# Optimization experiments

Measured on AMD Instinct MI355X. Metric: run time of the kernel, lower is better.

## Reference

```python
import jax, jax.numpy as jnp
import numpy as np

B, L, H, D = 4, 2048, 8, 64


def _combined_mask(Lq):
    # True = masked (disallowed), matching masked_fill_(mask, -inf)
    i = jnp.arange(Lq)[:, None]
    j = jnp.arange(Lq)[None, :]
    diff = i - j
    # log-sparse: query i attends to itself and positions at power-of-2 offsets back
    pow2 = (diff > 0) & ((diff & (diff - 1)) == 0)
    allowed = (diff == 0) | pow2
    log_mask = ~allowed
    causal = j > i  # TriangularCausalMask: strictly-upper triangle masked
    return log_mask | causal  # [Lq, Lq]


def setup_inputs() -> dict:
    key = jax.random.key(0)
    kq, kk, kv = jax.random.split(key, 3)
    return {
        "queries": jax.random.normal(kq, (B, L, H, D), jnp.float32),
        "keys": jax.random.normal(kk, (B, L, H, D), jnp.float32),
        "values": jax.random.normal(kv, (B, L, H, D), jnp.float32),
    }


def reference(queries, keys, values):
    Bq, Lq, Hh, Dd = queries.shape
    scale = 1.0 / jnp.sqrt(jnp.asarray(Dd, queries.dtype))
    # dense scores [B,H,L,L], then structured log-sparse + causal masking
    scores = jnp.einsum('blhd,bshd->bhls', queries, keys)
    mask = _combined_mask(Lq)  # [L,L] True = masked
    scores = jnp.where(mask[None, None, :, :], -jnp.inf, scores)
    A = jax.nn.softmax(scale * scores, axis=-1)  # scale*(-inf) stays -inf
    # dropout is identity in eval mode (reference baseline)
    V = jnp.einsum('bhls,bshd->blhd', A, values)
    return V
```

## Files before the change

kernel.cpp:

```cpp
#include <hip/hip_runtime.h>


typedef float f32x4 __attribute__((ext_vector_type(4)));

constexpr int B = 4, L = 2048, H = 8, D = 64;
constexpr int STRIP = 32, WIN = 32, LROWS = STRIP + WIN;
constexpr int NWG = B * H * (L / STRIP);

__global__ __launch_bounds__(256) void logsparse_attn_kernel(
    const float* __restrict__ Qg, const float* __restrict__ Kg,
    const float* __restrict__ Vg, float* __restrict__ Og) {
  __shared__ float Ks[LROWS * D];
  __shared__ float Vs[LROWS * D];

  const int bid   = blockIdx.x;
  const int xcd   = bid & 7;
  const int kk    = bid >> 3;
  const int bh    = xcd * 4 + (kk >> 6);
  const int strip = kk & 63;
  const int b = bh >> 3, h = bh & 7;
  const int s = strip * STRIP;

  const int tid  = threadIdx.x;
  const int w    = tid >> 6;
  const int lane = tid & 63;
  const int sub  = lane >> 4;
  const int dl   = lane & 15;

  f32x4 kreg[4], vreg[4];
  int dst[4];
  #pragma unroll
  for (int q = 0; q < 4; ++q) {
    const int r  = w * 16 + q * 4 + sub;
    const int j  = s - WIN + r;
    const int jc = j < 0 ? 0 : j;
    const uint32_t src = (((uint32_t)(b * L + jc)) * H + h) * D + dl * 4;
    kreg[q] = *(const f32x4*)(Kg + src);
    vreg[q] = *(const f32x4*)(Vg + src);
    dst[q]  = r * D + dl * 4;
  }
  #pragma unroll
  for (int q = 0; q < 4; ++q) {
    *(f32x4*)&Ks[dst[q]] = kreg[q];
    *(f32x4*)&Vs[dst[q]] = vreg[q];
  }
  __syncthreads();

  const float qs = 0.125f * 1.4426950408889634f;

  #pragma unroll
  for (int p = 0; p < 2; ++p) {
    const int il = w * 8 + p * 4 + sub;
    const int i  = s + il;
    const uint32_t qb = (((uint32_t)(b * L + i)) * H + h) * D + dl * 4;
    f32x4 q4 = *(const f32x4*)(Qg + qb);

    f32x4 kfar[5], vfar[5];
    #pragma unroll
    for (int t = 0; t < 5; ++t) {
      const int off = 64 << t;
      const int jc  = (off <= i) ? (i - off) : 0;
      const uint32_t rb = (((uint32_t)(b * L + jc)) * H + h) * D + dl * 4;
      kfar[t] = *(const f32x4*)(Kg + rb);
      vfar[t] = *(const f32x4*)(Vg + rb);
    }

    q4.x *= qs; q4.y *= qs; q4.z *= qs; q4.w *= qs;

    float sc[12];
    #pragma unroll
    for (int t = 0; t < 7; ++t) {
      const int off = (t == 0) ? 0 : (1 << (t - 1));
      const int r   = il + WIN - off;
      const f32x4 k4 = *(const f32x4*)&Ks[r * D + dl * 4];
      float pp = q4.x * k4.x + q4.y * k4.y + q4.z * k4.z + q4.w * k4.w;
      pp += __shfl_xor(pp, 1, 64);
      pp += __shfl_xor(pp, 2, 64);
      pp += __shfl_xor(pp, 4, 64);
      pp += __shfl_xor(pp, 8, 64);
      sc[t] = (off <= i) ? pp : -1e30f;
    }
    #pragma unroll
    for (int t = 0; t < 5; ++t) {
      const int off = 64 << t;
      float pp = q4.x * kfar[t].x + q4.y * kfar[t].y
               + q4.z * kfar[t].z + q4.w * kfar[t].w;
      pp += __shfl_xor(pp, 1, 64);
      pp += __shfl_xor(pp, 2, 64);
      pp += __shfl_xor(pp, 4, 64);
      pp += __shfl_xor(pp, 8, 64);
      sc[7 + t] = (off <= i) ? pp : -1e30f;
    }

    const float ma = fmaxf(fmaxf(sc[0], sc[1]), fmaxf(sc[2], sc[3]));
    const float mb = fmaxf(fmaxf(sc[4], sc[5]), fmaxf(sc[6], sc[7]));
    const float mc = fmaxf(fmaxf(sc[8], sc[9]), fmaxf(sc[10], sc[11]));
    const float m  = fmaxf(fmaxf(ma, mb), mc);
    #pragma unroll
    for (int t = 0; t < 12; ++t) sc[t] = __builtin_amdgcn_exp2f(sc[t] - m);
    const float sa = (sc[0] + sc[1]) + (sc[2] + sc[3]);
    const float sb = (sc[4] + sc[5]) + (sc[6] + sc[7]);
    const float sd = (sc[8] + sc[9]) + (sc[10] + sc[11]);
    const float inv = __builtin_amdgcn_rcpf(sa + sb + sd);

    f32x4 acc = {0.f, 0.f, 0.f, 0.f};
    #pragma unroll
    for (int t = 0; t < 7; ++t) {
      const int off = (t == 0) ? 0 : (1 << (t - 1));
      const int r   = il + WIN - off;
      const f32x4 v4 = *(const f32x4*)&Vs[r * D + dl * 4];
      acc.x += sc[t] * v4.x;  acc.y += sc[t] * v4.y;
      acc.z += sc[t] * v4.z;  acc.w += sc[t] * v4.w;
    }
    #pragma unroll
    for (int t = 0; t < 5; ++t) {
      acc.x += sc[7 + t] * vfar[t].x;  acc.y += sc[7 + t] * vfar[t].y;
      acc.z += sc[7 + t] * vfar[t].z;  acc.w += sc[7 + t] * vfar[t].w;
    }
    acc.x *= inv; acc.y *= inv; acc.z *= inv; acc.w *= inv;
    __builtin_nontemporal_store(acc, reinterpret_cast<f32x4*>(Og + qb));
  }
}

extern "C" void kernel_launch(void* const* d_in, const int* in_sizes, int n_in,
                              void* d_out, int out_size, void* d_ws, size_t ws_size,
                              hipStream_t stream) {
  const float* Q = (const float*)d_in[0];
  const float* K = (const float*)d_in[1];
  const float* V = (const float*)d_in[2];
  float* O = (float*)d_out;

  logsparse_attn_kernel<<<NWG, 256, 0, stream>>>(Q, K, V, O);
}
```

Baseline: 95.05 us.

## Store local K in fp16 LDS, use fdot2, remap lanes to 8 per row

Local-window K rows are converted to fp16 in LDS and the near-window dot products use packed fdot2. Lanes are remapped so each query row uses 8 lanes of 8 dims, which removes the two-pass loop and one shuffle stage per reduction. Far V loads are deferred until after the score computation, and launch bounds now request higher occupancy. The fp16 rounding of Q and K reduces precision for the local scores, while the far scores stay in fp32.

After: 93.93 us. About the same (-1.2%).

```diff
diff --git a/kernel.cpp b/kernel.cpp
--- a/kernel.cpp
+++ b/kernel.cpp
@@ -1,17 +1,19 @@
 #include <hip/hip_runtime.h>
 
 
-typedef float f32x4 __attribute__((ext_vector_type(4)));
+typedef float  f32x4 __attribute__((ext_vector_type(4)));
+typedef __fp16 f16x2 __attribute__((ext_vector_type(2)));
+typedef __fp16 f16x8 __attribute__((ext_vector_type(8)));
 
 constexpr int B = 4, L = 2048, H = 8, D = 64;
 constexpr int STRIP = 32, WIN = 32, LROWS = STRIP + WIN;
 constexpr int NWG = B * H * (L / STRIP);
 
-__global__ __launch_bounds__(256) void logsparse_attn_kernel(
+__global__ __launch_bounds__(256, 4) void logsparse_attn_kernel(
     const float* __restrict__ Qg, const float* __restrict__ Kg,
     const float* __restrict__ Vg, float* __restrict__ Og) {
-  __shared__ float Ks[LROWS * D];
-  __shared__ float Vs[LROWS * D];
+  __shared__ __fp16 Ksh[LROWS * D];
+  __shared__ float  Vsh[LROWS * D];
 
   const int bid   = blockIdx.x;
   const int xcd   = bid & 7;
@@ -24,102 +26,130 @@
   const int tid  = threadIdx.x;
   const int w    = tid >> 6;
   const int lane = tid & 63;
-  const int sub  = lane >> 4;
-  const int dl   = lane & 15;
+  const int g    = lane >> 3;
+  const int dl   = lane & 7;
 
-  f32x4 kreg[4], vreg[4];
-  int dst[4];
   #pragma unroll
-  for (int q = 0; q < 4; ++q) {
-    const int r  = w * 16 + q * 4 + sub;
-    const int j  = s - WIN + r;
+  for (int cc = 0; cc < 2; ++cc) {
+    const int c = tid + cc * 256;
+    const int r = c >> 3, part = c & 7;
+    const int j = s - WIN + r;
     const int jc = j < 0 ? 0 : j;
-    const uint32_t src = (((uint32_t)(b * L + jc)) * H + h) * D + dl * 4;
-    kreg[q] = *(const f32x4*)(Kg + src);
-    vreg[q] = *(const f32x4*)(Vg + src);
-    dst[q]  = r * D + dl * 4;
+    const float* src = Kg + (((uint32_t)(b * L + jc)) * H + h) * D + part * 8;
+    const f32x4 a0 = *(const f32x4*)src;
+    const f32x4 a1 = *(const f32x4*)(src + 4);
+    const f16x2 h0 = __builtin_amdgcn_cvt_pkrtz(a0.x, a0.y);
+    const f16x2 h1 = __builtin_amdgcn_cvt_pkrtz(a0.z, a0.w);
+    const f16x2 h2 = __builtin_amdgcn_cvt_pkrtz(a1.x, a1.y);
+    const f16x2 h3 = __builtin_amdgcn_cvt_pkrtz(a1.z, a1.w);
+    const f16x8 hv = {h0.x, h0.y, h1.x, h1.y, h2.x, h2.y, h3.x, h3.y};
+    *(f16x8*)&Ksh[r * D + part * 8] = hv;
   }
   #pragma unroll
-  for (int q = 0; q < 4; ++q) {
-    *(f32x4*)&Ks[dst[q]] = kreg[q];
-    *(f32x4*)&Vs[dst[q]] = vreg[q];
+  for (int cc = 0; cc < 4; ++cc) {
+    const int c = tid + cc * 256;
+    const int r = c >> 4, part = c & 15;
+    const int j = s - WIN + r;
+    const int jc = j < 0 ? 0 : j;
+    *(f32x4*)&Vsh[r * D + part * 4] =
+        *(const f32x4*)(Vg + (((uint32_t)(b * L + jc)) * H + h) * D + part * 4);
   }
   __syncthreads();
 
+  const int il = w * 8 + g;
+  const int i  = s + il;
+  const uint32_t qb = (((uint32_t)(b * L + i)) * H + h) * D + dl * 8;
+
+  f32x4 qa = *(const f32x4*)(Qg + qb);
+  f32x4 qc = *(const f32x4*)(Qg + qb + 4);
+
+  f32x4 kfa[5], kfb[5];
+  #pragma unroll
+  for (int t = 0; t < 5; ++t) {
+    const int off = 64 << t;
+    const int jc  = (off <= i) ? (i - off) : 0;
+    const float* rp = Kg + (((uint32_t)(b * L + jc)) * H + h) * D + dl * 8;
+    kfa[t] = *(const f32x4*)rp;
+    kfb[t] = *(const f32x4*)(rp + 4);
+  }
+
   const float qs = 0.125f * 1.4426950408889634f;
+  qa *= qs;  qc *= qs;
+  const f16x2 q01 = __builtin_amdgcn_cvt_pkrtz(qa.x, qa.y);
+  const f16x2 q23 = __builtin_amdgcn_cvt_pkrtz(qa.z, qa.w);
+  const f16x2 q45 = __builtin_amdgcn_cvt_pkrtz(qc.x, qc.y);
+  const f16x2 q67 = __builtin_amdgcn_cvt_pkrtz(qc.z, qc.w);
 
+  float sc[12];
   #pragma unroll
-  for (int p = 0; p < 2; ++p) {
-    const int il = w * 8 + p * 4 + sub;
-    const int i  = s + il;
-    const uint32_t qb = (((uint32_t)(b * L + i)) * H + h) * D + dl * 4;
-    f32x4 q4 = *(const f32x4*)(Qg + qb);
+  for (int t = 0; t < 7; ++t) {
+    const int off = (t == 0) ? 0 : (1 << (t - 1));
+    const int r   = il + WIN - off;
+    const f16x8 kv = *(const f16x8*)&Ksh[r * D + dl * 8];
+    const f16x2 k01 = {kv[0], kv[1]}, k23 = {kv[2], kv[3]};
+    const f16x2 k45 = {kv[4], kv[5]}, k67 = {kv[6], kv[7]};
+    float p = __builtin_amdgcn_fdot2(q01, k01, 0.f, false);
+    p = __builtin_amdgcn_fdot2(q23, k23, p, false);
+    p = __builtin_amdgcn_fdot2(q45, k45, p, false);
+    p = __builtin_amdgcn_fdot2(q67, k67, p, false);
+    p += __shfl_xor(p, 1, 64);
+    p += __shfl_xor(p, 2, 64);
+    p += __shfl_xor(p, 4, 64);
+    sc[t] = (off <= i) ? p : -1e30f;
+  }
+  #pragma unroll
+  for (int t = 0; t < 5; ++t) {
+    const int off = 64 << t;
+    float p = qa.x * kfa[t].x + qa.y * kfa[t].y
+            + qa.z * kfa[t].z + qa.w * kfa[t].w
+            + qc.x * kfb[t].x + qc.y * kfb[t].y
+            + qc.z * kfb[t].z + qc.w * kfb[t].w;
+    p += __shfl_xor(p, 1, 64);
+    p += __shfl_xor(p, 2, 64);
+    p += __shfl_xor(p, 4, 64);
+    sc[7 + t] = (off <= i) ? p : -1e30f;
+  }
 
-    f32x4 kfar[5], vfar[5];
-    #pragma unroll
-    for (int t = 0; t < 5; ++t) {
-      const int off = 64 << t;
-      const int jc  = (off <= i) ? (i - off) : 0;
-      const uint32_t rb = (((uint32_t)(b * L + jc)) * H + h) * D + dl * 4;
-      kfar[t] = *(const f32x4*)(Kg + rb);
-      vfar[t] = *(const f32x4*)(Vg + rb);
-    }
+  f32x4 vfa[5], vfb[5];
+  #pragma unroll
+  for (int t = 0; t < 5; ++t) {
+    const int off = 64 << t;
+    const int jc  = (off <= i) ? (i - off) : 0;
+    const float* vp = Vg + (((uint32_t)(b * L + jc)) * H + h) * D + dl * 8;
+    vfa[t] = *(const f32x4*)vp;
+    vfb[t] = *(const f32x4*)(vp + 4);
+  }
 
-    q4.x *= qs; q4.y *= qs; q4.z *= qs; q4.w *= qs;
+  const float ma = fmaxf(fmaxf(sc[0], sc[1]), fmaxf(sc[2], sc[3]));
+  const float mb = fmaxf(fmaxf(sc[4], sc[5]), fmaxf(sc[6], sc[7]));
+  const float mc = fmaxf(fmaxf(sc[8], sc[9]), fmaxf(sc[10], sc[11]));
+  const float m  = fmaxf(fmaxf(ma, mb), mc);
+  #pragma unroll
+  for (int t = 0; t < 12; ++t) sc[t] = __builtin_amdgcn_exp2f(sc[t] - m);
+  const float sa = (sc[0] + sc[1]) + (sc[2] + sc[3]);
+  const float sb = (sc[4] + sc[5]) + (sc[6] + sc[7]);
+  const float sd = (sc[8] + sc[9]) + (sc[10] + sc[11]);
+  const float inv = __builtin_amdgcn_rcpf(sa + sb + sd);
 
-    float sc[12];
-    #pragma unroll
-    for (int t = 0; t < 7; ++t) {
-      const int off = (t == 0) ? 0 : (1 << (t - 1));
-      const int r   = il + WIN - off;
-      const f32x4 k4 = *(const f32x4*)&Ks[r * D + dl * 4];
-      float pp = q4.x * k4.x + q4.y * k4.y + q4.z * k4.z + q4.w * k4.w;
-      pp += __shfl_xor(pp, 1, 64);
-      pp += __shfl_xor(pp, 2, 64);
-      pp += __shfl_xor(pp, 4, 64);
-      pp += __shfl_xor(pp, 8, 64);
-      sc[t] = (off <= i) ? pp : -1e30f;
-    }
-    #pragma unroll
-    for (int t = 0; t < 5; ++t) {
-      const int off = 64 << t;
-      float pp = q4.x * kfar[t].x + q4.y * kfar[t].y
-               + q4.z * kfar[t].z + q4.w * kfar[t].w;
-      pp += __shfl_xor(pp, 1, 64);
-      pp += __shfl_xor(pp, 2, 64);
-      pp += __shfl_xor(pp, 4, 64);
-      pp += __shfl_xor(pp, 8, 64);
-      sc[7 + t] = (off <= i) ? pp : -1e30f;
-    }
-
-    const float ma = fmaxf(fmaxf(sc[0], sc[1]), fmaxf(sc[2], sc[3]));
-    const float mb = fmaxf(fmaxf(sc[4], sc[5]), fmaxf(sc[6], sc[7]));
-    const float mc = fmaxf(fmaxf(sc[8], sc[9]), fmaxf(sc[10], sc[11]));
-    const float m  = fmaxf(fmaxf(ma, mb), mc);
-    #pragma unroll
-    for (int t = 0; t < 12; ++t) sc[t] = __builtin_amdgcn_exp2f(sc[t] - m);
-    const float sa = (sc[0] + sc[1]) + (sc[2] + sc[3]);
-    const float sb = (sc[4] + sc[5]) + (sc[6] + sc[7]);
-    const float sd = (sc[8] + sc[9]) + (sc[10] + sc[11]);
-    const float inv = __builtin_amdgcn_rcpf(sa + sb + sd);
-
-    f32x4 acc = {0.f, 0.f, 0.f, 0.f};
-    #pragma unroll
-    for (int t = 0; t < 7; ++t) {
-      const int off = (t == 0) ? 0 : (1 << (t - 1));
-      const int r   = il + WIN - off;
-      const f32x4 v4 = *(const f32x4*)&Vs[r * D + dl * 4];
-      acc.x += sc[t] * v4.x;  acc.y += sc[t] * v4.y;
-      acc.z += sc[t] * v4.z;  acc.w += sc[t] * v4.w;
-    }
-    #pragma unroll
-    for (int t = 0; t < 5; ++t) {
-      acc.x += sc[7 + t] * vfar[t].x;  acc.y += sc[7 + t] * vfar[t].y;
-      acc.z += sc[7 + t] * vfar[t].z;  acc.w += sc[7 + t] * vfar[t].w;
-    }
-    acc.x *= inv; acc.y *= inv; acc.z *= inv; acc.w *= inv;
-    __builtin_nontemporal_store(acc, reinterpret_cast<f32x4*>(Og + qb));
+  f32x4 aa = {0.f, 0.f, 0.f, 0.f};
+  f32x4 ab = {0.f, 0.f, 0.f, 0.f};
+  #pragma unroll
+  for (int t = 0; t < 7; ++t) {
+    const int off = (t == 0) ? 0 : (1 << (t - 1));
+    const int r   = il + WIN - off;
+    const f32x4 v0 = *(const f32x4*)&Vsh[r * D + dl * 8];
+    const f32x4 v1 = *(const f32x4*)&Vsh[r * D + dl * 8 + 4];
+    aa += sc[t] * v0;
+    ab += sc[t] * v1;
   }
+  #pragma unroll
+  for (int t = 0; t < 5; ++t) {
+    aa += sc[7 + t] * vfa[t];
+    ab += sc[7 + t] * vfb[t];
+  }
+  aa *= inv;  ab *= inv;
+  __builtin_nontemporal_store(aa, reinterpret_cast<f32x4*>(Og + qb));
+  __builtin_nontemporal_store(ab, reinterpret_cast<f32x4*>(Og + qb + 4));
 }
 
 extern "C" void kernel_launch(void* const* d_in, const int* in_sizes, int n_in,
```
